# Kernel tuning notes

Hardware: AMD Instinct MI355X
Metric: run time of the kernel (lower is better)

## Reference

```python
import jax, jax.numpy as jnp
import numpy as np
import math

L = 4      # model_layers
D = 512    # model_filters
H = 32     # heads = max(D//16, 1)
DH = D // H  # 16
S = 1024   # dataset_dimension == max_len == seq_len
B = 2
EPS = 1e-5


def setup_inputs() -> dict:
    key = jax.random.key(0)
    ks = jax.random.split(key, 12)
    scale = 0.02
    n = lambda k, shape: jax.random.normal(k, shape, dtype=jnp.float32) * scale
    return {
        "x": jax.random.normal(ks[0], (B, S), dtype=jnp.float32),
        "Winit": n(ks[1], (D,)),               # init_linear weight (1->D)
        "binit": jnp.zeros((D,), jnp.float32),
        "Wq": n(ks[2], (L, D, D)), "bq": jnp.zeros((L, D), jnp.float32),
        "Wk": n(ks[3], (L, D, D)), "bk": jnp.zeros((L, D), jnp.float32),
        "Wv": n(ks[4], (L, D, D)), "bv": jnp.zeros((L, D), jnp.float32),
        "Er": jax.random.normal(ks[5], (L, S, DH), dtype=jnp.float32) * scale,
        "Wlin": n(ks[6], (L, D, D)), "blin": jnp.zeros((L, D), jnp.float32),
        "ln_g": jnp.ones((L, D), jnp.float32), "ln_b": jnp.zeros((L, D), jnp.float32),
        "Wout": n(ks[7], (D, 1)),              # output_linear, no bias
    }


def layernorm(x, g, b):
    mu = jnp.mean(x, axis=-1, keepdims=True)
    var = jnp.mean(jnp.square(x - mu), axis=-1, keepdims=True)
    return (x - mu) * jax.lax.rsqrt(var + EPS) * g + b


def rel_attn(h, Wq, bq, Wk, bk, Wv, bv, Er):
    # h: [B, S, D]
    b_, s_, _ = h.shape
    q = (h @ Wq + bq).reshape(b_, s_, H, DH).transpose(0, 2, 1, 3)  # [B,H,S,dh]
    k = (h @ Wk + bk).reshape(b_, s_, H, DH).transpose(0, 2, 1, 3)
    v = (h @ Wv + bv).reshape(b_, s_, H, DH).transpose(0, 2, 1, 3)
    # relative-position term with skew trick (seq_len == max_len -> full Er)
    QEr = jnp.einsum('bhsd,td->bhst', q, Er)                  # [B,H,S,S]
    padded = jnp.pad(QEr, ((0, 0), (0, 0), (0, 0), (1, 0)))   # pad left of last dim
    Srel = padded.reshape(b_, H, s_ + 1, s_)[:, :, 1:, :]     # skew
    scores = (jnp.einsum('bhsd,bhtd->bhst', q, k) + Srel) / math.sqrt(DH)
    mask = jnp.tril(jnp.ones((s_, s_), dtype=bool))           # causal
    scores = jnp.where(mask, scores, -jnp.inf)
    p = jax.nn.softmax(scores, axis=-1)
    o = jnp.einsum('bhst,bhtd->bhsd', p, v)
    return o.transpose(0, 2, 1, 3).reshape(b_, s_, D)


def reference(x, Winit, binit, Wq, bq, Wk, bk, Wv, bv, Er, Wlin, blin, ln_g, ln_b, Wout):
    # init_linear(1->D) on scalar per position, then exact gelu
    h = jax.nn.gelu(x[..., None] * Winit + binit, approximate=False)  # [B,S,D]
    for l in range(L):
        a = rel_attn(h, Wq[l], bq[l], Wk[l], bk[l], Wv[l], bv[l], Er[l])
        y = layernorm(a @ Wlin[l] + blin[l], ln_g[l], ln_b[l])
        h = h + jax.nn.gelu(y, approximate=False)
    return h.sum(axis=-2) @ Wout  # [B,1]
```

## Files before the change

### kernel.cpp

```cpp
#include <hip/hip_runtime.h>
#include <math.h>

#define NL 4
#define DIM 512
#define NH 32
#define DHD 16
#define SEQ 1024
#define NB 2
#define LN_EPS 1e-5f
#define NEGF (-1e30f)
#define QSC 0.36067376022224085f

typedef _Float16 half4 __attribute__((ext_vector_type(4)));
typedef _Float16 half8 __attribute__((ext_vector_type(8)));
typedef float floatx4 __attribute__((ext_vector_type(4)));

__device__ __forceinline__ float gelu_exact(float x) {
    return 0.5f * x * (1.0f + erff(x * 0.70710678118654752f));
}

__device__ __forceinline__ void async16(const void* g, void* l) {
    __builtin_amdgcn_global_load_lds(
        (const __attribute__((address_space(1))) void*)g,
        (__attribute__((address_space(3))) void*)l, 16, 0, 0);
}

__global__ __launch_bounds__(256) void k_prep_all(const float* __restrict__ Wq,
        const float* __restrict__ Wk, const float* __restrict__ Wv,
        const float* __restrict__ Wlin, const float* __restrict__ bq,
        const float* __restrict__ bk, const float* __restrict__ bv,
        const float* __restrict__ Er, const float* __restrict__ x,
        const float* __restrict__ Wi, const float* __restrict__ bi,
        _Float16* __restrict__ Wqkvt, _Float16* __restrict__ Wlint,
        float* __restrict__ bqkv, _Float16* __restrict__ Erh,
        float* __restrict__ h, _Float16* __restrict__ hf) {
    __shared__ _Float16 lt[64][72];
    const int u = blockIdx.x;
    const int tid = threadIdx.x;
    if (u < 1024) {
        const int kx = u & 7, ny = (u >> 3) & 7, mz = u >> 6;
        const int l = mz >> 2, which = mz & 3;
        const float* src = (which == 0) ? Wq : (which == 1) ? Wk : (which == 2) ? Wv : Wlin;
        src += (size_t)l * 262144;
        const float scale = (which == 0) ? QSC : 1.0f;
        _Float16* dst = (which < 3) ? (Wqkvt + (size_t)l * 786432 + (size_t)which * 262144)
                                    : (Wlint + (size_t)l * 262144);
        const int k0 = kx << 6, n0 = ny << 6;
        #pragma unroll
        for (int p = 0; p < 4; p++) {
            int kl = (p << 4) + (tid >> 4);
            int n4 = (tid & 15) << 2;
            float4 wv = *(const float4*)(src + (size_t)(k0 + kl) * 512 + n0 + n4);
            lt[n4 + 0][kl] = (_Float16)(wv.x * scale);
            lt[n4 + 1][kl] = (_Float16)(wv.y * scale);
            lt[n4 + 2][kl] = (_Float16)(wv.z * scale);
            lt[n4 + 3][kl] = (_Float16)(wv.w * scale);
        }
        __syncthreads();
        int nl = tid >> 2, k16 = (tid & 3) << 4;
        float4* d4 = (float4*)(dst + (size_t)(n0 + nl) * 512 + k0 + k16);
        const float4* s4 = (const float4*)&lt[nl][k16];
        d4[0] = s4[0];
        d4[1] = s4[1];
    } else if (u < 2048) {
        int idx0 = ((u - 1024) << 10) + (tid << 2);
        int d = idx0 & 511, bs = idx0 >> 9;
        float xs = x[bs];
        float4 wv = *(const float4*)(Wi + d);
        float4 bv = *(const float4*)(bi + d);
        float4 r;
        r.x = gelu_exact(xs * wv.x + bv.x);
        r.y = gelu_exact(xs * wv.y + bv.y);
        r.z = gelu_exact(xs * wv.z + bv.z);
        r.w = gelu_exact(xs * wv.w + bv.w);
        *(float4*)(h + idx0) = r;
        half4 rh = {(_Float16)r.x, (_Float16)r.y, (_Float16)r.z, (_Float16)r.w};
        *(half4*)(hf + idx0) = rh;
    } else {
        int idx = ((u - 2048) << 8) + tid;
        if (idx < NL * 1536) {
            int l = idx / 1536, j = idx % 1536;
            int which = j >> 9, jj = j & 511;
            float val = (which == 0) ? bq[l * 512 + jj] * QSC
                      : (which == 1) ? bk[l * 512 + jj] : bv[l * 512 + jj];
            bqkv[idx] = val;
        }
        int e = idx - NL * 1536;
        if (e >= 0 && e < NL * SEQ * DHD) Erh[e] = (_Float16)Er[e];
    }
}

__global__ __launch_bounds__(256) void k_gemm_qkv(const _Float16* __restrict__ A,
        const _Float16* __restrict__ Bt, const float* __restrict__ bias,
        _Float16* __restrict__ o16) {
    __shared__ _Float16 As[2][128][32];
    __shared__ _Float16 Bs[2][96][32];
    const int tid = threadIdx.x;
    const int w = tid >> 6, lane = tid & 63;
    const int nn = lane & 15, qd = lane >> 4;
    const int wm = (w & 1) << 6;
    const int wn = (w >> 1) * 48;
    const int m0 = blockIdx.x << 7;
    const int n0 = blockIdx.y * 96;
    const int srow = lane >> 2, scol = (lane & 3) << 3;
    floatx4 acc[4][3] = {};
    for (int k0 = 0; k0 < 512; k0 += 64) {
        __syncthreads();
        #pragma unroll
        for (int p = 0; p < 2; p++) {
            #pragma unroll
            for (int hh = 0; hh < 2; hh++)
                async16(A + (size_t)(m0 + (hh << 6) + (w << 4) + srow) * 512
                          + k0 + (p << 5) + scol,
                        &As[p][(hh << 6) + (w << 4)][0]);
            async16(Bt + (size_t)(n0 + (w << 4) + srow) * 512 + k0 + (p << 5) + scol,
                    &Bs[p][(w << 4)][0]);
            if (w < 2)
                async16(Bt + (size_t)(n0 + 64 + (w << 4) + srow) * 512
                           + k0 + (p << 5) + scol,
                        &Bs[p][64 + (w << 4)][0]);
        }
        __syncthreads();
        #pragma unroll
        for (int ks = 0; ks < 2; ks++) {
            half8 af[4], bf[3];
            #pragma unroll
            for (int t = 0; t < 4; t++)
                af[t] = *(const half8*)&As[ks][wm + (t << 4) + nn][qd << 3];
            #pragma unroll
            for (int t = 0; t < 3; t++)
                bf[t] = *(const half8*)&Bs[ks][wn + (t << 4) + nn][qd << 3];
            #pragma unroll
            for (int ti = 0; ti < 4; ti++)
                #pragma unroll
                for (int tj = 0; tj < 3; tj++)
                    acc[ti][tj] = __builtin_amdgcn_mfma_f32_16x16x32_f16(
                            af[ti], bf[tj], acc[ti][tj], 0, 0, 0);
        }
    }
    float bv3[3];
    #pragma unroll
    for (int tj = 0; tj < 3; tj++) bv3[tj] = bias[n0 + wn + (tj << 4) + nn];
    #pragma unroll
    for (int ti = 0; ti < 4; ti++) {
        int rg = m0 + wm + (ti << 4) + (qd << 2);
        #pragma unroll
        for (int tj = 0; tj < 3; tj++) {
            int colg = n0 + wn + (tj << 4) + nn;
            int which = colg >> 9, ci = colg & 511;
            _Float16* op = o16 + (size_t)which * 1048576 + (size_t)rg * 512 + ci;
            #pragma unroll
            for (int r = 0; r < 4; r++)
                op[(size_t)r * 512] = (_Float16)(acc[ti][tj][r] + bv3[tj]);
        }
    }
}

__global__ __launch_bounds__(256) void k_gemm_lin(const _Float16* __restrict__ A,
        const _Float16* __restrict__ Bt, const float* __restrict__ bias,
        float* __restrict__ y) {
    __shared__ _Float16 As[2 * 64 * 32];
    __shared__ _Float16 Bs[2 * 64 * 32];
    const int tid = threadIdx.x;
    const int w = tid >> 6, lane = tid & 63;
    const int nn = lane & 15, qd = lane >> 4;
    const int wm = (w & 1) << 5, wn = (w >> 1) << 5;
    const int m0 = blockIdx.x << 6, n0 = blockIdx.y << 6;
    const int l2r = lane >> 2, l2c = (lane & 3) << 3;
    const _Float16* Ag = A + (size_t)(m0 + (w << 4) + l2r) * 512 + l2c;
    const _Float16* Bg = Bt + (size_t)(n0 + (w << 4) + l2r) * 512 + l2c;
    _Float16* Al = As + (w << 9);
    _Float16* Bl = Bs + (w << 9);
    floatx4 acc[2][2] = {};
    for (int k0 = 0; k0 < 512; k0 += 64) {
        __syncthreads();
        #pragma unroll
        for (int p = 0; p < 2; p++) {
            async16(Ag + k0 + (p << 5), Al + (p << 11));
            async16(Bg + k0 + (p << 5), Bl + (p << 11));
        }
        __syncthreads();
        #pragma unroll
        for (int ks = 0; ks < 2; ks++) {
            half8 af[2], bf[2];
            #pragma unroll
            for (int t = 0; t < 2; t++) {
                af[t] = *(const half8*)&As[(ks << 11) + ((wm + (t << 4) + nn) << 5) + (qd << 3)];
                bf[t] = *(const half8*)&Bs[(ks << 11) + ((wn + (t << 4) + nn) << 5) + (qd << 3)];
            }
            #pragma unroll
            for (int ti = 0; ti < 2; ti++)
                #pragma unroll
                for (int tj = 0; tj < 2; tj++)
                    acc[ti][tj] = __builtin_amdgcn_mfma_f32_16x16x32_f16(
                            af[ti], bf[tj], acc[ti][tj], 0, 0, 0);
        }
    }
    float bv2[2];
    #pragma unroll
    for (int tj = 0; tj < 2; tj++) bv2[tj] = bias[n0 + wn + (tj << 4) + nn];
    #pragma unroll
    for (int ti = 0; ti < 2; ti++) {
        int rg = m0 + wm + (ti << 4) + (qd << 2);
        #pragma unroll
        for (int tj = 0; tj < 2; tj++) {
            int colg = n0 + wn + (tj << 4) + nn;
            float* op = y + (size_t)rg * 512 + colg;
            #pragma unroll
            for (int r = 0; r < 4; r++)
                op[(size_t)r * 512] = acc[ti][tj][r] + bv2[tj];
        }
    }
}

__global__ __launch_bounds__(256, 4) void k_attn_mfma(const _Float16* __restrict__ q,
        const _Float16* __restrict__ k, const _Float16* __restrict__ v,
        const _Float16* __restrict__ Er, _Float16* __restrict__ aout) {
    __shared__ _Float16 Ks[256][20];
    __shared__ _Float16 Vts[16][268];
    __shared__ float Rel[4][16][80];
    const int tid = threadIdx.x;
    const int wid = tid >> 6, lane = tid & 63;
    const int nn = lane & 15, a4 = (lane >> 4) << 2;
    const int b_ = blockIdx.x >> 5, h_ = blockIdx.x & 31;
    const int y = blockIdx.y;
    const int t_ = tid >> 2, c4 = (tid & 3) << 2;
    const int r0p[2] = {64 * y, 64 * (15 - y)};
    const int R = r0p[1] + 64;

    half4 qf[2];
    floatx4 O[2];
    float m[2], lsum[2];
    #pragma unroll
    for (int ph = 0; ph < 2; ph++) {
        int s0w = r0p[ph] + (wid << 4);
        qf[ph] = *(const half4*)(q + ((size_t)(b_ * SEQ + s0w + nn)) * DIM + h_ * DHD + a4);
        O[ph] = (floatx4){0.f, 0.f, 0.f, 0.f};
        m[ph] = NEGF;
        lsum[ph] = 0.f;
    }

    for (int part = 0; part < 4; part++) {
        const int p0 = part << 8;
        if (p0 >= R) break;
        const int pend = (R < p0 + 256) ? R : (p0 + 256);
        __syncthreads();
        const int ng = (pend - p0) >> 6;
        for (int g = 0; g < ng; g++) {
            int rl = (g << 6) + t_;
            size_t gb = ((size_t)(b_ * SEQ + p0 + rl)) * DIM + h_ * DHD + c4;
            *(half4*)&Ks[rl][c4] = *(const half4*)(k + gb);
            half4 vv4 = *(const half4*)(v + gb);
            Vts[c4 + 0][rl] = vv4.x;
            Vts[c4 + 1][rl] = vv4.y;
            Vts[c4 + 2][rl] = vv4.z;
            Vts[c4 + 3][rl] = vv4.w;
        }
        __syncthreads();
        #pragma unroll
        for (int ph = 0; ph < 2; ph++) {
            const int r0 = r0p[ph];
            const int s0w = r0 + (wid << 4);
            const int hi = (r0 + 64 < pend) ? (r0 + 64) : pend;
            for (int ct = p0; ct < hi; ct += 64) {
                const int ctl = ct - p0;
                const int jbw = 1008 - s0w + ct;
                #pragma unroll
                for (int jt = 0; jt < 5; jt++) {
                    int j = jbw + (jt << 4) + nn;
                    j = (j < SEQ - 1) ? j : (SEQ - 1);
                    half4 ef = *(const half4*)(Er + (size_t)j * DHD + a4);
                    floatx4 racc = {0.f, 0.f, 0.f, 0.f};
                    racc = __builtin_amdgcn_mfma_f32_16x16x16f16(ef, qf[ph], racc, 0, 0, 0);
                    *(floatx4*)&Rel[wid][nn][(jt << 4) + a4] = racc;
                }
                float st[4][4];
                const bool diag = (ct == r0);
                #pragma unroll
                for (int tt = 0; tt < 4; tt++) {
                    half4 kf = *(const half4*)&Ks[ctl + (tt << 4) + nn][a4];
                    floatx4 sacc = {0.f, 0.f, 0.f, 0.f};
                    sacc = __builtin_amdgcn_mfma_f32_16x16x16f16(kf, qf[ph], sacc, 0, 0, 0);
                    const float* rp = &Rel[wid][nn][15 - nn + (tt << 4) + a4];
                    #pragma unroll
                    for (int r = 0; r < 4; r++) {
                        int tl = (tt << 4) + a4 + r;
                        float sv = sacc[r] + rp[r];
                        if (diag && (tl > (wid << 4) + nn)) sv = NEGF;
                        st[tt][r] = sv;
                    }
                }
                float cmax = NEGF;
                #pragma unroll
                for (int tt = 0; tt < 4; tt++)
                    #pragma unroll
                    for (int r = 0; r < 4; r++) cmax = fmaxf(cmax, st[tt][r]);
                cmax = fmaxf(cmax, __shfl_xor(cmax, 16));
                cmax = fmaxf(cmax, __shfl_xor(cmax, 32));
                float mnew = fmaxf(m[ph], cmax);
                float alpha = exp2f(m[ph] - mnew);
                m[ph] = mnew;
                float csum = 0.f;
                half4 pf[4];
                #pragma unroll
                for (int tt = 0; tt < 4; tt++) {
                    float p0e = exp2f(st[tt][0] - mnew);
                    float p1e = exp2f(st[tt][1] - mnew);
                    float p2e = exp2f(st[tt][2] - mnew);
                    float p3e = exp2f(st[tt][3] - mnew);
                    csum += (p0e + p1e) + (p2e + p3e);
                    half4 ph4 = {(_Float16)p0e, (_Float16)p1e, (_Float16)p2e, (_Float16)p3e};
                    pf[tt] = ph4;
                }
                lsum[ph] = lsum[ph] * alpha + csum;
                O[ph][0] *= alpha; O[ph][1] *= alpha; O[ph][2] *= alpha; O[ph][3] *= alpha;
                #pragma unroll
                for (int tt = 0; tt < 4; tt++) {
                    half4 vf = *(const half4*)&Vts[nn][ctl + (tt << 4) + a4];
                    O[ph] = __builtin_amdgcn_mfma_f32_16x16x16f16(vf, pf[tt], O[ph], 0, 0, 0);
                }
            }
        }
    }
    #pragma unroll
    for (int ph = 0; ph < 2; ph++) {
        float lt = lsum[ph];
        lt += __shfl_xor(lt, 16);
        lt += __shfl_xor(lt, 32);
        float linv = 1.0f / lt;
        int s0w = r0p[ph] + (wid << 4);
        half4 ov = { (_Float16)(O[ph][0] * linv), (_Float16)(O[ph][1] * linv),
                     (_Float16)(O[ph][2] * linv), (_Float16)(O[ph][3] * linv) };
        *(half4*)(aout + ((size_t)(b_ * SEQ + s0w + nn)) * DIM + h_ * DHD + a4) = ov;
    }
}

__global__ __launch_bounds__(256) void k_ln_gelu_res(const float* __restrict__ y,
        const float* __restrict__ gam, const float* __restrict__ bet,
        float* __restrict__ h, _Float16* __restrict__ hf) {
    int row = (blockIdx.x << 2) + (threadIdx.x >> 6);
    int lane = threadIdx.x & 63;
    const float* yr = y + (size_t)row * DIM + (lane << 3);
    float4 v0 = *(const float4*)(yr);
    float4 v1 = *(const float4*)(yr + 4);
    float sum = (v0.x + v0.y) + (v0.z + v0.w) + (v1.x + v1.y) + (v1.z + v1.w);
    float sq = v0.x*v0.x + v0.y*v0.y + v0.z*v0.z + v0.w*v0.w
             + v1.x*v1.x + v1.y*v1.y + v1.z*v1.z + v1.w*v1.w;
    #pragma unroll
    for (int off = 32; off > 0; off >>= 1) {
        sum += __shfl_xor(sum, off);
        sq  += __shfl_xor(sq, off);
    }
    float mu = sum * (1.0f / DIM);
    float var = sq * (1.0f / DIM) - mu * mu;
    float rs = rsqrtf(var + LN_EPS);
    float4 g0 = *(const float4*)(gam + (lane << 3));
    float4 g1 = *(const float4*)(gam + (lane << 3) + 4);
    float4 b0 = *(const float4*)(bet + (lane << 3));
    float4 b1 = *(const float4*)(bet + (lane << 3) + 4);
    float* hr = h + (size_t)row * DIM + (lane << 3);
    float4 h0 = *(const float4*)(hr);
    float4 h1 = *(const float4*)(hr + 4);
    float o[8];
    o[0] = h0.x + gelu_exact((v0.x - mu) * rs * g0.x + b0.x);
    o[1] = h0.y + gelu_exact((v0.y - mu) * rs * g0.y + b0.y);
    o[2] = h0.z + gelu_exact((v0.z - mu) * rs * g0.z + b0.z);
    o[3] = h0.w + gelu_exact((v0.w - mu) * rs * g0.w + b0.w);
    o[4] = h1.x + gelu_exact((v1.x - mu) * rs * g1.x + b1.x);
    o[5] = h1.y + gelu_exact((v1.y - mu) * rs * g1.y + b1.y);
    o[6] = h1.z + gelu_exact((v1.z - mu) * rs * g1.z + b1.z);
    o[7] = h1.w + gelu_exact((v1.w - mu) * rs * g1.w + b1.w);
    *(float4*)(hr)     = make_float4(o[0], o[1], o[2], o[3]);
    *(float4*)(hr + 4) = make_float4(o[4], o[5], o[6], o[7]);
    half8 oh = {(_Float16)o[0], (_Float16)o[1], (_Float16)o[2], (_Float16)o[3],
                (_Float16)o[4], (_Float16)o[5], (_Float16)o[6], (_Float16)o[7]};
    *(half8*)(hf + (size_t)row * DIM + (lane << 3)) = oh;
}

__global__ __launch_bounds__(256) void k_colsum1(const float* __restrict__ h,
        float* __restrict__ pa) {
    int bt = blockIdx.x;
    int base = bt << 3;
    int tid = threadIdx.x;
    #pragma unroll
    for (int half = 0; half < 2; half++) {
        int d = (half << 8) + tid;
        float acc = 0.f;
        #pragma unroll
        for (int i = 0; i < 8; i++)
            acc += h[(size_t)(base + i) * DIM + d];
        pa[(size_t)bt * DIM + d] = acc;
    }
}

__global__ __launch_bounds__(256) void k_colsum2(const float* __restrict__ pa,
        float* __restrict__ pb) {
    __shared__ float red[4][64];
    int b = blockIdx.x, dt = blockIdx.y;
    int tid = threadIdx.x;
    int c = tid & 63, ig = tid >> 6;
    int d = (dt << 6) + c;
    float s = 0.f;
    for (int i = ig; i < 128; i += 4)
        s += pa[(size_t)(b * 128 + i) * DIM + d];
    red[ig][c] = s;
    __syncthreads();
    if (ig == 0)
        pb[(size_t)b * DIM + d] = red[0][c] + red[1][c] + red[2][c] + red[3][c];
}

__global__ __launch_bounds__(256) void k_final(const float* __restrict__ pb,
        const float* __restrict__ Wout, float* __restrict__ out) {
    __shared__ float red[4][2];
    int tid = threadIdx.x;
    float acc0 = 0.f, acc1 = 0.f;
    #pragma unroll
    for (int half = 0; half < 2; half++) {
        int d = (half << 8) + tid;
        float w = Wout[d];
        acc0 += pb[d] * w;
        acc1 += pb[DIM + d] * w;
    }
    #pragma unroll
    for (int off = 32; off > 0; off >>= 1) {
        acc0 += __shfl_down(acc0, off);
        acc1 += __shfl_down(acc1, off);
    }
    if ((tid & 63) == 0) { red[tid >> 6][0] = acc0; red[tid >> 6][1] = acc1; }
    __syncthreads();
    if (tid == 0) {
        out[0] = red[0][0] + red[1][0] + red[2][0] + red[3][0];
        out[1] = red[0][1] + red[1][1] + red[2][1] + red[3][1];
    }
}

extern "C" void kernel_launch(void* const* d_in, const int* in_sizes, int n_in,
                              void* d_out, int out_size, void* d_ws, size_t ws_size,
                              hipStream_t stream) {
    const float* x    = (const float*)d_in[0];
    const float* Wi   = (const float*)d_in[1];
    const float* bi   = (const float*)d_in[2];
    const float* Wq   = (const float*)d_in[3];
    const float* bq   = (const float*)d_in[4];
    const float* Wk   = (const float*)d_in[5];
    const float* bk   = (const float*)d_in[6];
    const float* Wv   = (const float*)d_in[7];
    const float* bv   = (const float*)d_in[8];
    const float* Er   = (const float*)d_in[9];
    const float* Wlin = (const float*)d_in[10];
    const float* blin = (const float*)d_in[11];
    const float* lng  = (const float*)d_in[12];
    const float* lnb  = (const float*)d_in[13];
    const float* Wout = (const float*)d_in[14];
    float* out = (float*)d_out;

    float* ws = (float*)d_ws;
    const size_t N1 = 1048576;
    float*     h     = ws;
    _Float16*  hf    = (_Float16*)(ws + N1);
    _Float16*  qh    = (_Float16*)(ws + N1 + N1/2);
    _Float16*  ah    = (_Float16*)(ws + 3 * N1);
    float*     y     = ws + 3 * N1 + N1/2;
    _Float16*  Wqkvt = (_Float16*)(ws + 4 * N1 + N1/2);
    _Float16*  Wlint = (_Float16*)(ws + 6 * N1);
    float*     bqkv  = ws + 6 * N1 + N1/2;
    _Float16*  Erh   = (_Float16*)(ws + 6 * N1 + N1/2 + 8192);
    float*     pa    = ws + 6 * N1 + N1/2 + 8192 + 32768;
    float*     pb    = pa + 131072;

    k_prep_all<<<dim3(2328), dim3(256), 0, stream>>>(Wq, Wk, Wv, Wlin, bq, bk, bv,
            Er, x, Wi, bi, Wqkvt, Wlint, bqkv, Erh, h, hf);
    for (int l = 0; l < NL; l++) {
        k_gemm_qkv<<<dim3(16, 16), dim3(256), 0, stream>>>(
                hf, Wqkvt + (size_t)l * 786432, bqkv + l * 1536, qh);
        k_attn_mfma<<<dim3(NB * NH, 8), dim3(256), 0, stream>>>(
                qh, qh + 1048576, qh + 2097152, Erh + (size_t)l * 16384, ah);
        k_gemm_lin<<<dim3(32, 8), dim3(256), 0, stream>>>(
                ah, Wlint + (size_t)l * 262144, blin + l * 512, y);
        k_ln_gelu_res<<<dim3(512), dim3(256), 0, stream>>>(
                y, lng + l * 512, lnb + l * 512, h, hf);
    }
    k_colsum1<<<dim3(256), dim3(256), 0, stream>>>(h, pa);
    k_colsum2<<<dim3(2, 8), dim3(256), 0, stream>>>(pa, pb);
    k_final<<<dim3(1), dim3(256), 0, stream>>>(pb, Wout, out);
}
```

Before: 323.1 us.

## Split attention key tiles across two wave groups and merge softmax partials

Result: faster. 300.8 us (-6.9%).

```diff
diff --git a/kernel.cpp b/kernel.cpp
--- a/kernel.cpp
+++ b/kernel.cpp
@@ -213,18 +213,18 @@
     }
 }
 
-__global__ __launch_bounds__(256, 4) void k_attn_mfma(const _Float16* __restrict__ q,
+__global__ __launch_bounds__(512) void k_attn_mfma(const _Float16* __restrict__ q,
         const _Float16* __restrict__ k, const _Float16* __restrict__ v,
         const _Float16* __restrict__ Er, _Float16* __restrict__ aout) {
     __shared__ _Float16 Ks[256][20];
     __shared__ _Float16 Vts[16][268];
-    __shared__ float Rel[4][16][80];
+    __shared__ float Rel[8][16][84];
     const int tid = threadIdx.x;
-    const int wid = tid >> 6, lane = tid & 63;
+    const int w = tid >> 6, lane = tid & 63;
+    const int wg = w & 3, half = w >> 2;
     const int nn = lane & 15, a4 = (lane >> 4) << 2;
     const int b_ = blockIdx.x >> 5, h_ = blockIdx.x & 31;
     const int y = blockIdx.y;
-    const int t_ = tid >> 2, c4 = (tid & 3) << 2;
     const int r0p[2] = {64 * y, 64 * (15 - y)};
     const int R = r0p[1] + 64;
 
@@ -233,7 +233,7 @@
     float m[2], lsum[2];
     #pragma unroll
     for (int ph = 0; ph < 2; ph++) {
-        int s0w = r0p[ph] + (wid << 4);
+        int s0w = r0p[ph] + (wg << 4);
         qf[ph] = *(const half4*)(q + ((size_t)(b_ * SEQ + s0w + nn)) * DIM + h_ * DHD + a4);
         O[ph] = (floatx4){0.f, 0.f, 0.f, 0.f};
         m[ph] = NEGF;
@@ -245,24 +245,29 @@
         if (p0 >= R) break;
         const int pend = (R < p0 + 256) ? R : (p0 + 256);
         __syncthreads();
-        const int ng = (pend - p0) >> 6;
-        for (int g = 0; g < ng; g++) {
-            int rl = (g << 6) + t_;
-            size_t gb = ((size_t)(b_ * SEQ + p0 + rl)) * DIM + h_ * DHD + c4;
-            *(half4*)&Ks[rl][c4] = *(const half4*)(k + gb);
-            half4 vv4 = *(const half4*)(v + gb);
-            Vts[c4 + 0][rl] = vv4.x;
-            Vts[c4 + 1][rl] = vv4.y;
-            Vts[c4 + 2][rl] = vv4.z;
-            Vts[c4 + 3][rl] = vv4.w;
+        {
+            int rl0 = tid >> 2, c4 = (tid & 3) << 2;
+            for (int g = 0; g < pend - p0; g += 128) {
+                int rl = g + rl0;
+                if (rl < pend - p0) {
+                    size_t gb = ((size_t)(b_ * SEQ + p0 + rl)) * DIM + h_ * DHD + c4;
+                    *(half4*)&Ks[rl][c4] = *(const half4*)(k + gb);
+                    half4 vv4 = *(const half4*)(v + gb);
+                    Vts[c4 + 0][rl] = vv4.x;
+                    Vts[c4 + 1][rl] = vv4.y;
+                    Vts[c4 + 2][rl] = vv4.z;
+                    Vts[c4 + 3][rl] = vv4.w;
+                }
+            }
         }
         __syncthreads();
         #pragma unroll
         for (int ph = 0; ph < 2; ph++) {
             const int r0 = r0p[ph];
-            const int s0w = r0 + (wid << 4);
+            const int s0w = r0 + (wg << 4);
             const int hi = (r0 + 64 < pend) ? (r0 + 64) : pend;
             for (int ct = p0; ct < hi; ct += 64) {
+                if (((ct >> 6) & 1) != half) continue;
                 const int ctl = ct - p0;
                 const int jbw = 1008 - s0w + ct;
                 #pragma unroll
@@ -272,7 +277,7 @@
                     half4 ef = *(const half4*)(Er + (size_t)j * DHD + a4);
                     floatx4 racc = {0.f, 0.f, 0.f, 0.f};
                     racc = __builtin_amdgcn_mfma_f32_16x16x16f16(ef, qf[ph], racc, 0, 0, 0);
-                    *(floatx4*)&Rel[wid][nn][(jt << 4) + a4] = racc;
+                    *(floatx4*)&Rel[w][nn][(jt << 4) + a4] = racc;
                 }
                 float st[4][4];
                 const bool diag = (ct == r0);
@@ -281,12 +286,12 @@
                     half4 kf = *(const half4*)&Ks[ctl + (tt << 4) + nn][a4];
                     floatx4 sacc = {0.f, 0.f, 0.f, 0.f};
                     sacc = __builtin_amdgcn_mfma_f32_16x16x16f16(kf, qf[ph], sacc, 0, 0, 0);
-                    const float* rp = &Rel[wid][nn][15 - nn + (tt << 4) + a4];
+                    const float* rp = &Rel[w][nn][15 - nn + (tt << 4) + a4];
                     #pragma unroll
                     for (int r = 0; r < 4; r++) {
                         int tl = (tt << 4) + a4 + r;
                         float sv = sacc[r] + rp[r];
-                        if (diag && (tl > (wid << 4) + nn)) sv = NEGF;
+                        if (diag && (tl > (wg << 4) + nn)) sv = NEGF;
                         st[tt][r] = sv;
                     }
                 }
@@ -322,16 +327,42 @@
             }
         }
     }
-    #pragma unroll
-    for (int ph = 0; ph < 2; ph++) {
-        float lt = lsum[ph];
-        lt += __shfl_xor(lt, 16);
-        lt += __shfl_xor(lt, 32);
-        float linv = 1.0f / lt;
-        int s0w = r0p[ph] + (wid << 4);
-        half4 ov = { (_Float16)(O[ph][0] * linv), (_Float16)(O[ph][1] * linv),
-                     (_Float16)(O[ph][2] * linv), (_Float16)(O[ph][3] * linv) };
-        *(half4*)(aout + ((size_t)(b_ * SEQ + s0w + nn)) * DIM + h_ * DHD + a4) = ov;
+    float* mb = (float*)Rel;
+    __syncthreads();
+    if (half == 1) {
+        #pragma unroll
+        for (int ph = 0; ph < 2; ph++) {
+            int base = (((wg << 1) + ph) << 6) + lane;
+            mb[base]        = O[ph][0];
+            mb[base + 1024] = O[ph][1];
+            mb[base + 2048] = O[ph][2];
+            mb[base + 3072] = O[ph][3];
+            mb[base + 4096] = m[ph];
+            mb[base + 5120] = lsum[ph];
+        }
+    }
+    __syncthreads();
+    if (half == 0) {
+        #pragma unroll
+        for (int ph = 0; ph < 2; ph++) {
+            int base = (((wg << 1) + ph) << 6) + lane;
+            float m1 = mb[base + 4096];
+            float l1 = mb[base + 5120];
+            float mm = fmaxf(m[ph], m1);
+            float a0 = exp2f(m[ph] - mm);
+            float a1 = exp2f(m1 - mm);
+            float lt = lsum[ph] * a0 + l1 * a1;
+            lt += __shfl_xor(lt, 16);
+            lt += __shfl_xor(lt, 32);
+            float linv = 1.0f / lt;
+            float o0 = (O[ph][0] * a0 + mb[base]        * a1) * linv;
+            float o1 = (O[ph][1] * a0 + mb[base + 1024] * a1) * linv;
+            float o2 = (O[ph][2] * a0 + mb[base + 2048] * a1) * linv;
+            float o3 = (O[ph][3] * a0 + mb[base + 3072] * a1) * linv;
+            int s0w = r0p[ph] + (wg << 4);
+            half4 ov = {(_Float16)o0, (_Float16)o1, (_Float16)o2, (_Float16)o3};
+            *(half4*)(aout + ((size_t)(b_ * SEQ + s0w + nn)) * DIM + h_ * DHD + a4) = ov;
+        }
     }
 }
 
@@ -473,7 +504,7 @@
     for (int l = 0; l < NL; l++) {
         k_gemm_qkv<<<dim3(16, 16), dim3(256), 0, stream>>>(
                 hf, Wqkvt + (size_t)l * 786432, bqkv + l * 1536, qh);
-        k_attn_mfma<<<dim3(NB * NH, 8), dim3(256), 0, stream>>>(
+        k_attn_mfma<<<dim3(NB * NH, 8), dim3(512), 0, stream>>>(
                 qh, qh + 1048576, qh + 2097152, Erh + (size_t)l * 16384, ah);
         k_gemm_lin<<<dim3(32, 8), dim3(256), 0, stream>>>(
                 ah, Wlint + (size_t)l * 262144, blin + l * 512, y);
```
